# Performance work log

Hardware: AMD Instinct MI355X
Metric: run time of the kernel (lower is better)

The kernel has to match this reference:

```python
import jax, jax.numpy as jnp
import numpy as np

B, PS, H, W = 32, 1536, 32, 64
TNS = H * W                 # total_num_selects = 2048
NJ = TNS // 16              # num_joints = 128
QK = PS // 4                # q/k channels = 384
NC = 200                    # num_classes
BN_EPS = 1e-5


def setup_inputs() -> dict:
    key = jax.random.key(0)
    ks = jax.random.split(key, 8)
    s = 0.02  # small init scale for weights
    inp = {
        "x": jax.random.normal(ks[0], (B, PS, H, W), jnp.float32),
        # param_pool0: Linear(TNS -> NJ)
        "w_pool0": jax.random.normal(ks[1], (NJ, TNS), jnp.float32) * s,
        "b_pool0": jnp.zeros((NJ,), jnp.float32),
        # learnable adjacency: eye/100 + 1/100
        "adj1": jnp.eye(NJ, dtype=jnp.float32) / 100.0 + 1.0 / 100.0,
        # conv_q1 / conv_k1: Conv1d(PS -> PS//4, kernel=1)
        "w_q": jax.random.normal(ks[2], (QK, PS), jnp.float32) * s,
        "b_q": jnp.zeros((QK,), jnp.float32),
        "w_k": jax.random.normal(ks[3], (QK, PS), jnp.float32) * s,
        "b_k": jnp.zeros((QK,), jnp.float32),
        # alpha1 (torch inits to 0; we use 0.1 so attention branch has nonzero effect/grads)
        "alpha": jnp.array([0.1], jnp.float32),
        # conv1: Conv1d(PS -> PS, kernel=1)
        "w_c1": jax.random.normal(ks[4], (PS, PS), jnp.float32) * s,
        "b_c1": jnp.zeros((PS,), jnp.float32),
        # batch_norm1 affine params
        "gamma": jnp.ones((PS,), jnp.float32),
        "beta": jnp.zeros((PS,), jnp.float32),
        # param_pool1: Linear(NJ -> 1)
        "w_pool1": jax.random.normal(ks[5], (1, NJ), jnp.float32) * s,
        "b_pool1": jnp.zeros((1,), jnp.float32),
        # classifier: Linear(PS -> NC)
        "w_cls": jax.random.normal(ks[6], (NC, PS), jnp.float32) * s,
        "b_cls": jnp.zeros((NC,), jnp.float32),
    }
    return inp


def reference(x, w_pool0, b_pool0, adj1, w_q, b_q, w_k, b_k, alpha,
              w_c1, b_c1, gamma, beta, w_pool1, b_pool1, w_cls, b_cls):
    b, c = x.shape[0], x.shape[1]
    hs = x.reshape(b, c, -1)                                   # (B, PS, TNS)
    # param_pool0: pool selects down to joints
    hs = jnp.einsum('bcs,js->bcj', hs, w_pool0) + b_pool0      # (B, PS, NJ)
    # 1x1-conv q/k then mean over channel dim
    q1 = (jnp.einsum('oc,bcj->boj', w_q, hs) + b_q[:, None]).mean(axis=1)  # (B, NJ)
    k1 = (jnp.einsum('oc,bcj->boj', w_k, hs) + b_k[:, None]).mean(axis=1)  # (B, NJ)
    # outer-difference attention, tanh-bounded, blended with learnable adjacency
    A1 = adj1 + jnp.tanh(q1[:, :, None] - k1[:, None, :]) * alpha[0]       # (B, NJ, NJ)
    # conv1 (1x1) then adjacency-weighted matmul
    hs = jnp.einsum('oc,bcj->boj', w_c1, hs) + b_c1[:, None]   # (B, PS, NJ)
    hs = jnp.einsum('bcj,bjk->bck', hs, A1)                    # (B, PS, NJ)
    # BatchNorm1d over (batch, joints) per channel (training-mode batch stats)
    mean = hs.mean(axis=(0, 2))
    var = hs.var(axis=(0, 2))
    hs = (hs - mean[None, :, None]) * jax.lax.rsqrt(var + BN_EPS)[None, :, None]
    hs = gamma[None, :, None] * hs + beta[None, :, None]
    # param_pool1 (NJ -> 1), dropout is identity in eval, flatten, classify
    hs = jnp.einsum('bcj,j->bc', hs, w_pool1[0]) + b_pool1[0]  # (B, PS)
    out = hs @ w_cls.T + b_cls                                 # (B, NC)
    return out
```

## Files before the change

kernel.cpp:

```cpp
#include <hip/hip_runtime.h>
#include <hip/hip_bf16.h>

#define B_ 32
#define PS_ 1536
#define TNS_ 2048
#define NJ_ 128
#define QK_ 384
#define NC_ 200
#define BN_EPS_ 1e-5f

typedef __attribute__((ext_vector_type(8))) short short8;
typedef __attribute__((ext_vector_type(4))) float float4v;
typedef unsigned short ushort_t;

__device__ __forceinline__ unsigned short f2b(float f) {
    unsigned int u = __float_as_uint(f);
    return (unsigned short)((u + 0x7FFFu + ((u >> 16) & 1u)) >> 16);
}
__device__ __forceinline__ float b2f_lo(unsigned int u) { return __uint_as_float(u << 16); }
__device__ __forceinline__ float b2f_hi(unsigned int u) { return __uint_as_float(u & 0xffff0000u); }

__device__ __forceinline__ void mma_chunk(const short* As, const short* Bs,
                                          int wm, int wn, int lane, float4v acc[4][4]) {
    const int m0 = wm + (lane & 15);
    const int n0 = wn + (lane & 15);
    const int quad = lane >> 4;
    #pragma unroll
    for (int kk = 0; kk < 64; kk += 32) {
        short8 a[4], b[4];
        const int kb = quad * 8 + kk;
        #pragma unroll
        for (int i = 0; i < 4; ++i) {
            a[i] = *(const short8*)&As[(m0 + i * 16) * 72 + kb];
            b[i] = *(const short8*)&Bs[(n0 + i * 16) * 72 + kb];
        }
        #pragma unroll
        for (int i = 0; i < 4; ++i)
            #pragma unroll
            for (int j = 0; j < 4; ++j)
                acc[i][j] = __builtin_amdgcn_mfma_f32_16x16x32_bf16(a[i], b[j], acc[i][j], 0, 0, 0);
    }
}

__device__ __forceinline__ void stage_f32(const float* __restrict__ src, size_t stride,
                                          short* dst, int tid) {
    #pragma unroll
    for (int p = 0; p < 8; ++p) {
        int r = (tid >> 4) + p * 16;
        int kq = (tid & 15) * 4;
        float4 v = *(const float4*)(src + (size_t)r * stride + kq);
        ushort4 u = { f2b(v.x), f2b(v.y), f2b(v.z), f2b(v.w) };
        *(ushort4*)&dst[r * 72 + kq] = u;
    }
}
__device__ __forceinline__ void stage_b16(const ushort_t* __restrict__ src, size_t stride,
                                          short* dst, int tid) {
    #pragma unroll
    for (int p = 0; p < 4; ++p) {
        int r = (tid >> 3) + p * 32;
        int kq = (tid & 7) * 8;
        uint4 v = *(const uint4*)(src + (size_t)r * stride + kq);
        *(uint4*)&dst[r * 72 + kq] = v;
    }
}

__global__ void k_prep_all(const float* __restrict__ wq, const float* __restrict__ bq,
                           const float* __restrict__ wk, const float* __restrict__ bk,
                           const float* __restrict__ wp1,
                           const float* __restrict__ w0, const float* __restrict__ wc1,
                           float* __restrict__ wqb, float* __restrict__ wkb,
                           float* __restrict__ scal,
                           float* __restrict__ bnsum, float* __restrict__ bnsq,
                           ushort_t* __restrict__ w0b, ushort_t* __restrict__ wc1b) {
    const int blk = blockIdx.x;
    const int tid = threadIdx.x;
    if (blk < 6) {
        int c = blk * 256 + tid;
        float s = 0.f;
        for (int o = 0; o < QK_; ++o) s += wq[(size_t)o * PS_ + c];
        wqb[c] = s * (1.0f / QK_);
        bnsum[c] = 0.f; bnsq[c] = 0.f;
    } else if (blk < 12) {
        int c = (blk - 6) * 256 + tid;
        float s = 0.f;
        for (int o = 0; o < QK_; ++o) s += wk[(size_t)o * PS_ + c];
        wkb[c] = s * (1.0f / QK_);
    } else if (blk == 12) {
        __shared__ float red[256];
        float s = (tid < QK_ ? bq[tid] : 0.f) + (tid + 256 < QK_ ? bq[tid + 256] : 0.f);
        red[tid] = s; __syncthreads();
        for (int off = 128; off > 0; off >>= 1) { if (tid < off) red[tid] += red[tid + off]; __syncthreads(); }
        if (tid == 0) scal[0] = red[0] * (1.0f / QK_);
        __syncthreads();
        s = (tid < QK_ ? bk[tid] : 0.f) + (tid + 256 < QK_ ? bk[tid + 256] : 0.f);
        red[tid] = s; __syncthreads();
        for (int off = 128; off > 0; off >>= 1) { if (tid < off) red[tid] += red[tid + off]; __syncthreads(); }
        if (tid == 0) scal[1] = red[0] * (1.0f / QK_);
        __syncthreads();
        s = (tid < NJ_ ? wp1[tid] : 0.f);
        red[tid] = s; __syncthreads();
        for (int off = 128; off > 0; off >>= 1) { if (tid < off) red[tid] += red[tid + off]; __syncthreads(); }
        if (tid == 0) scal[2] = red[0];
    } else if (blk < 269) {
        int i = (blk - 13) * 256 + tid;
        float4 v = ((const float4*)w0)[i];
        ushort4 u = { f2b(v.x), f2b(v.y), f2b(v.z), f2b(v.w) };
        ((ushort4*)w0b)[i] = u;
    } else {
        int i = (blk - 269) * 256 + tid;
        float4 v = ((const float4*)wc1)[i];
        ushort4 u = { f2b(v.x), f2b(v.y), f2b(v.z), f2b(v.w) };
        ((ushort4*)wc1b)[i] = u;
    }
}

__global__ __launch_bounds__(256) void k_gemm1(const float* __restrict__ x,
        const ushort_t* __restrict__ w0b, const float* __restrict__ b0,
        ushort_t* __restrict__ hsT) {
    __shared__ __align__(16) short As[128 * 72];
    __shared__ __align__(16) short Bs[128 * 72];
    const int tid = threadIdx.x, lane = tid & 63, wave = tid >> 6;
    const int wm = (wave >> 1) * 64, wn = (wave & 1) * 64;
    const size_t m0 = (size_t)blockIdx.x * 128;
    float4v acc[4][4] = {};
    for (int k0 = 0; k0 < TNS_; k0 += 64) {
        stage_f32(x + m0 * TNS_ + k0, TNS_, As, tid);
        stage_b16(w0b + k0, TNS_, Bs, tid);
        __syncthreads();
        mma_chunk(As, Bs, wm, wn, lane, acc);
        __syncthreads();
    }
    const int b = blockIdx.x / 12, cb = (blockIdx.x % 12) * 128;
    const int quad = lane >> 4;
    #pragma unroll
    for (int jn = 0; jn < 4; ++jn) {
        int j = wn + jn * 16 + (lane & 15);
        float bj = b0[j];
        #pragma unroll
        for (int im = 0; im < 4; ++im) {
            int c = cb + wm + im * 16 + quad * 4;
            float4v v = acc[im][jn];
            ushort4 u = { f2b(v[0] + bj), f2b(v[1] + bj), f2b(v[2] + bj), f2b(v[3] + bj) };
            *(ushort4*)&hsT[((size_t)(b * NJ_ + j)) * PS_ + c] = u;
        }
    }
}

__global__ __launch_bounds__(256) void k_q1k1(const ushort_t* __restrict__ hsT,
        const float* __restrict__ wqb, const float* __restrict__ wkb,
        float* __restrict__ q1, float* __restrict__ k1) {
    int wid = blockIdx.x * 4 + (threadIdx.x >> 6);
    int lane = threadIdx.x & 63;
    int b = wid >> 7, j = wid & 127;
    const unsigned int* row = (const unsigned int*)(hsT + ((size_t)(b * NJ_ + j)) * PS_);
    float sq = 0.f, sk = 0.f;
    #pragma unroll
    for (int i = 0; i < 12; ++i) {
        unsigned int u = row[i * 64 + lane];
        int c = (i * 64 + lane) * 2;
        float v0 = b2f_lo(u), v1 = b2f_hi(u);
        sq += wqb[c] * v0 + wqb[c + 1] * v1;
        sk += wkb[c] * v0 + wkb[c + 1] * v1;
    }
    #pragma unroll
    for (int off = 32; off > 0; off >>= 1) { sq += __shfl_down(sq, off, 64); sk += __shfl_down(sk, off, 64); }
    if (lane == 0) { q1[b * NJ_ + j] = sq; k1[b * NJ_ + j] = sk; }
}

__global__ void k_a1(const float* __restrict__ adj, const float* __restrict__ q1,
                     const float* __restrict__ k1, const float* __restrict__ alpha,
                     const float* __restrict__ scal, ushort_t* __restrict__ A1t) {
    int idx = blockIdx.x * 256 + threadIdx.x;
    int b = idx >> 14;
    int r = idx & 16383;
    int j2 = r >> 7;
    int j = r & 127;
    float dbias = scal[0] - scal[1];
    float t = tanhf(q1[b * NJ_ + j] - k1[b * NJ_ + j2] + dbias);
    A1t[idx] = f2b(adj[j * NJ_ + j2] + t * alpha[0]);
}

__global__ __launch_bounds__(256) void k_gemm23(const ushort_t* __restrict__ wc1b,
        const float* __restrict__ bc1, const ushort_t* __restrict__ hsT,
        const ushort_t* __restrict__ A1t, ushort_t* __restrict__ hs3b,
        float* __restrict__ bnsum, float* __restrict__ bnsq) {
    __shared__ __align__(16) short sm[2][128 * 72];
    __shared__ float bns_s[NJ_], bnq_s[NJ_];
    const int tid = threadIdx.x, lane = tid & 63, wave = tid >> 6;
    const int wm = (wave >> 1) * 64, wn = (wave & 1) * 64;
    const int b = blockIdx.y, ob = blockIdx.x * 128;
    if (tid < NJ_) { bns_s[tid] = 0.f; bnq_s[tid] = 0.f; }
    float4v acc[4][4] = {};
    const ushort_t* Abase = wc1b + (size_t)ob * PS_;
    const ushort_t* Bbase = hsT + (size_t)b * NJ_ * PS_;
    for (int k0 = 0; k0 < PS_; k0 += 64) {
        stage_b16(Abase + k0, PS_, sm[0], tid);
        stage_b16(Bbase + k0, PS_, sm[1], tid);
        __syncthreads();
        mma_chunk(sm[0], sm[1], wm, wn, lane, acc);
        __syncthreads();
    }
    short* C1 = &sm[0][0];
    const int quad = lane >> 4;
    #pragma unroll
    for (int im = 0; im < 4; ++im) {
        int o0l = wm + im * 16 + quad * 4;
        float bc[4] = { bc1[ob + o0l], bc1[ob + o0l + 1], bc1[ob + o0l + 2], bc1[ob + o0l + 3] };
        #pragma unroll
        for (int jn = 0; jn < 4; ++jn) {
            int j = wn + jn * 16 + (lane & 15);
            float4v v = acc[im][jn];
            #pragma unroll
            for (int r = 0; r < 4; ++r)
                C1[(o0l + r) * 136 + j] = (short)f2b(v[r] + bc[r]);
        }
    }
    __syncthreads();
    float4v acc2[4][4] = {};
    const ushort_t* Ap = A1t + (size_t)b * NJ_ * NJ_;
    const int m0 = wm + (lane & 15), n0 = wn + (lane & 15);
    #pragma unroll
    for (int kk = 0; kk < 128; kk += 32) {
        short8 a[4], bf[4];
        const int kb = quad * 8 + kk;
        #pragma unroll
        for (int i = 0; i < 4; ++i) a[i] = *(const short8*)&C1[(m0 + i * 16) * 136 + kb];
        #pragma unroll
        for (int j = 0; j < 4; ++j) bf[j] = *(const short8*)&Ap[(size_t)(n0 + j * 16) * NJ_ + kb];
        #pragma unroll
        for (int i = 0; i < 4; ++i)
            #pragma unroll
            for (int j = 0; j < 4; ++j)
                acc2[i][j] = __builtin_amdgcn_mfma_f32_16x16x32_bf16(a[i], bf[j], acc2[i][j], 0, 0, 0);
    }
    float s_[4][4] = {}, q_[4][4] = {};
    #pragma unroll
    for (int im = 0; im < 4; ++im) {
        int c0l = wm + im * 16 + quad * 4;
        #pragma unroll
        for (int jn = 0; jn < 4; ++jn) {
            int j2 = wn + jn * 16 + (lane & 15);
            float4v v = acc2[im][jn];
            #pragma unroll
            for (int r = 0; r < 4; ++r) {
                unsigned short us = f2b(v[r]);
                float vr = b2f_lo((unsigned int)us);
                s_[im][r] += vr; q_[im][r] += vr * vr;
                hs3b[((size_t)(b * PS_) + ob + c0l + r) * NJ_ + j2] = us;
            }
        }
    }
    #pragma unroll
    for (int m = 1; m < 16; m <<= 1) {
        #pragma unroll
        for (int im = 0; im < 4; ++im)
            #pragma unroll
            for (int r = 0; r < 4; ++r) {
                s_[im][r] += __shfl_xor(s_[im][r], m, 64);
                q_[im][r] += __shfl_xor(q_[im][r], m, 64);
            }
    }
    if ((lane & 15) == 0) {
        #pragma unroll
        for (int im = 0; im < 4; ++im)
            #pragma unroll
            for (int r = 0; r < 4; ++r) {
                int cl = wm + im * 16 + quad * 4 + r;
                atomicAdd(&bns_s[cl], s_[im][r]);
                atomicAdd(&bnq_s[cl], q_[im][r]);
            }
    }
    __syncthreads();
    if (tid < NJ_) {
        atomicAdd(&bnsum[ob + tid], bns_s[tid]);
        atomicAdd(&bnsq[ob + tid], bnq_s[tid]);
    }
}

__global__ void k_pool(const ushort_t* __restrict__ hs3b, const float* __restrict__ bnsum,
                       const float* __restrict__ bnsq, const float* __restrict__ gamma,
                       const float* __restrict__ beta, const float* __restrict__ wp1,
                       const float* __restrict__ bp1, const float* __restrict__ scal,
                       float* __restrict__ p) {
    int gid = blockIdx.x * 256 + threadIdx.x;
    int row = gid >> 6;
    int lane = gid & 63;
    int c = row % PS_;
    const unsigned int* hp = (const unsigned int*)(hs3b + (size_t)row * NJ_);
    unsigned int u = hp[lane];
    float d = wp1[2 * lane] * b2f_lo(u) + wp1[2 * lane + 1] * b2f_hi(u);
    #pragma unroll
    for (int off = 32; off > 0; off >>= 1) d += __shfl_down(d, off, 64);
    if (lane == 0) {
        float mean = bnsum[c] * (1.0f / 4096.0f);
        float var = bnsq[c] * (1.0f / 4096.0f) - mean * mean;
        float s = gamma[c] * rsqrtf(var + BN_EPS_);
        p[row] = s * d + (beta[c] - s * mean) * scal[2] + bp1[0];
    }
}

__global__ void k_cls(const float* __restrict__ p, const float* __restrict__ wcls,
                      const float* __restrict__ bcls, float* __restrict__ out) {
    int gid = blockIdx.x * 256 + threadIdx.x;
    int w = gid >> 6;
    int lane = gid & 63;
    int b = w / 200, n = w % 200;
    const float* pp = p + (size_t)b * PS_;
    const float* wp = wcls + (size_t)n * PS_;
    float s = 0.f;
    for (int c = lane; c < PS_; c += 64) s += pp[c] * wp[c];
    #pragma unroll
    for (int off = 32; off > 0; off >>= 1) s += __shfl_down(s, off, 64);
    if (lane == 0) out[w] = s + bcls[n];
}

extern "C" void kernel_launch(void* const* d_in, const int* in_sizes, int n_in,
                              void* d_out, int out_size, void* d_ws, size_t ws_size,
                              hipStream_t stream) {
    const float* x       = (const float*)d_in[0];
    const float* w_pool0 = (const float*)d_in[1];
    const float* b_pool0 = (const float*)d_in[2];
    const float* adj1    = (const float*)d_in[3];
    const float* w_q     = (const float*)d_in[4];
    const float* b_q     = (const float*)d_in[5];
    const float* w_k     = (const float*)d_in[6];
    const float* b_k     = (const float*)d_in[7];
    const float* alpha   = (const float*)d_in[8];
    const float* w_c1    = (const float*)d_in[9];
    const float* b_c1    = (const float*)d_in[10];
    const float* gamma   = (const float*)d_in[11];
    const float* beta    = (const float*)d_in[12];
    const float* w_pool1 = (const float*)d_in[13];
    const float* b_pool1 = (const float*)d_in[14];
    const float* w_cls   = (const float*)d_in[15];
    const float* b_cls   = (const float*)d_in[16];
    float* out = (float*)d_out;

    ushort_t* hsT  = (ushort_t*)d_ws;
    ushort_t* hs2  = hsT + 6291456;
    ushort_t* hs3b = hs2 + 6291456;
    ushort_t* w0b  = hs3b + 6291456;
    ushort_t* wc1b = w0b + 262144;
    ushort_t* A1t  = wc1b + 2359296;
    float* fb    = (float*)(A1t + 524288);
    float* wqb   = fb;
    float* wkb   = wqb + 1536;
    float* scal  = wkb + 1536;
    float* q1    = scal + 16;
    float* k1    = q1 + 4096;
    float* bnsum = k1 + 4096;
    float* bnsq  = bnsum + 1536;
    float* pbuf  = bnsq + 1536;
    size_t need = 44040192u + (size_t)(1536 + 1536 + 16 + 4096 + 4096 + 1536 + 1536 + 49152) * 4;
    if (ws_size < need) return;

    k_prep_all<<<2573, 256, 0, stream>>>(w_q, b_q, w_k, b_k, w_pool1, w_pool0, w_c1,
                                         wqb, wkb, scal, bnsum, bnsq, w0b, wc1b);
    k_gemm1 <<<384, 256, 0, stream>>>(x, w0b, b_pool0, hsT);
    k_q1k1  <<<1024, 256, 0, stream>>>(hsT, wqb, wkb, q1, k1);
    k_a1    <<<2048, 256, 0, stream>>>(adj1, q1, k1, alpha, scal, A1t);
    k_gemm23<<<dim3(12, 32), 256, 0, stream>>>(wc1b, b_c1, hsT, A1t, hs3b, bnsum, bnsq);
    k_pool  <<<12288, 256, 0, stream>>>(hs3b, bnsum, bnsq, gamma, beta, w_pool1, b_pool1, scal, pbuf);
    k_cls   <<<1600, 256, 0, stream>>>(pbuf, w_cls, b_cls, out);
}
```

Before: 677.6 us.

## Fuse q/k reduction into gemm1 and pooling into gemm23, use 512-thread blocks

The q1/k1 channel-mean dot products move into the gemm1 epilogue, accumulated with atomics into buffers that the prep kernel now zeroes. The wp1-weighted pooling moves into the gemm23 epilogue, so the bf16 hs3 tensor is no longer written and read back, and the BN affine is applied inside the classifier. Both GEMMs now launch 8 waves per block with a 4x2 MFMA tile per wave, halving each wave's accumulator footprint. In exchange, the q1/k1 sums become atomic-order nondeterministic and k_cls recomputes the BN scale for every output.

```diff
diff --git a/kernel.cpp b/kernel.cpp
--- a/kernel.cpp
+++ b/kernel.cpp
@@ -20,44 +20,43 @@
 __device__ __forceinline__ float b2f_lo(unsigned int u) { return __uint_as_float(u << 16); }
 __device__ __forceinline__ float b2f_hi(unsigned int u) { return __uint_as_float(u & 0xffff0000u); }
 
-__device__ __forceinline__ void mma_chunk(const short* As, const short* Bs,
-                                          int wm, int wn, int lane, float4v acc[4][4]) {
+__device__ __forceinline__ void mma_chunk42(const short* As, const short* Bs,
+                                            int wm, int wn, int lane, float4v acc[4][2]) {
     const int m0 = wm + (lane & 15);
     const int n0 = wn + (lane & 15);
     const int quad = lane >> 4;
     #pragma unroll
     for (int kk = 0; kk < 64; kk += 32) {
-        short8 a[4], b[4];
+        short8 a[4], b[2];
         const int kb = quad * 8 + kk;
         #pragma unroll
-        for (int i = 0; i < 4; ++i) {
-            a[i] = *(const short8*)&As[(m0 + i * 16) * 72 + kb];
-            b[i] = *(const short8*)&Bs[(n0 + i * 16) * 72 + kb];
-        }
+        for (int i = 0; i < 4; ++i) a[i] = *(const short8*)&As[(m0 + i * 16) * 72 + kb];
+        #pragma unroll
+        for (int j = 0; j < 2; ++j) b[j] = *(const short8*)&Bs[(n0 + j * 16) * 72 + kb];
         #pragma unroll
         for (int i = 0; i < 4; ++i)
             #pragma unroll
-            for (int j = 0; j < 4; ++j)
+            for (int j = 0; j < 2; ++j)
                 acc[i][j] = __builtin_amdgcn_mfma_f32_16x16x32_bf16(a[i], b[j], acc[i][j], 0, 0, 0);
     }
 }
 
-__device__ __forceinline__ void stage_f32(const float* __restrict__ src, size_t stride,
-                                          short* dst, int tid) {
-    #pragma unroll
-    for (int p = 0; p < 8; ++p) {
-        int r = (tid >> 4) + p * 16;
+__device__ __forceinline__ void stage_f32_512(const float* __restrict__ src, size_t stride,
+                                              short* dst, int tid) {
+    #pragma unroll
+    for (int p = 0; p < 4; ++p) {
+        int r = (tid >> 4) + p * 32;
         int kq = (tid & 15) * 4;
         float4 v = *(const float4*)(src + (size_t)r * stride + kq);
         ushort4 u = { f2b(v.x), f2b(v.y), f2b(v.z), f2b(v.w) };
         *(ushort4*)&dst[r * 72 + kq] = u;
     }
 }
-__device__ __forceinline__ void stage_b16(const ushort_t* __restrict__ src, size_t stride,
-                                          short* dst, int tid) {
-    #pragma unroll
-    for (int p = 0; p < 4; ++p) {
-        int r = (tid >> 3) + p * 32;
+__device__ __forceinline__ void stage_b16_512(const ushort_t* __restrict__ src, size_t stride,
+                                              short* dst, int tid) {
+    #pragma unroll
+    for (int p = 0; p < 2; ++p) {
+        int r = (tid >> 3) + p * 64;
         int kq = (tid & 7) * 8;
         uint4 v = *(const uint4*)(src + (size_t)r * stride + kq);
         *(uint4*)&dst[r * 72 + kq] = v;
@@ -71,6 +70,7 @@
                            float* __restrict__ wqb, float* __restrict__ wkb,
                            float* __restrict__ scal,
                            float* __restrict__ bnsum, float* __restrict__ bnsq,
+                           float* __restrict__ q1, float* __restrict__ k1,
                            ushort_t* __restrict__ w0b, ushort_t* __restrict__ wc1b) {
     const int blk = blockIdx.x;
     const int tid = threadIdx.x;
@@ -106,65 +106,70 @@
         float4 v = ((const float4*)w0)[i];
         ushort4 u = { f2b(v.x), f2b(v.y), f2b(v.z), f2b(v.w) };
         ((ushort4*)w0b)[i] = u;
-    } else {
+    } else if (blk < 2573) {
         int i = (blk - 269) * 256 + tid;
         float4 v = ((const float4*)wc1)[i];
         ushort4 u = { f2b(v.x), f2b(v.y), f2b(v.z), f2b(v.w) };
         ((ushort4*)wc1b)[i] = u;
-    }
-}
-
-__global__ __launch_bounds__(256) void k_gemm1(const float* __restrict__ x,
+    } else {
+        int i = (blk - 2573) * 256 + tid;
+        if (i < 4096) q1[i] = 0.f; else k1[i - 4096] = 0.f;
+    }
+}
+
+__global__ __launch_bounds__(512) void k_gemm1(const float* __restrict__ x,
         const ushort_t* __restrict__ w0b, const float* __restrict__ b0,
-        ushort_t* __restrict__ hsT) {
+        const float* __restrict__ wqb, const float* __restrict__ wkb,
+        ushort_t* __restrict__ hsT, float* __restrict__ q1, float* __restrict__ k1) {
     __shared__ __align__(16) short As[128 * 72];
     __shared__ __align__(16) short Bs[128 * 72];
     const int tid = threadIdx.x, lane = tid & 63, wave = tid >> 6;
-    const int wm = (wave >> 1) * 64, wn = (wave & 1) * 64;
-    const size_t m0 = (size_t)blockIdx.x * 128;
-    float4v acc[4][4] = {};
+    const int wm = (wave >> 2) * 64, wn = (wave & 3) * 32;
+    const size_t m0r = (size_t)blockIdx.x * 128;
+    float4v acc[4][2] = {};
     for (int k0 = 0; k0 < TNS_; k0 += 64) {
-        stage_f32(x + m0 * TNS_ + k0, TNS_, As, tid);
-        stage_b16(w0b + k0, TNS_, Bs, tid);
-        __syncthreads();
-        mma_chunk(As, Bs, wm, wn, lane, acc);
+        stage_f32_512(x + m0r * TNS_ + k0, TNS_, As, tid);
+        stage_b16_512(w0b + k0, TNS_, Bs, tid);
+        __syncthreads();
+        mma_chunk42(As, Bs, wm, wn, lane, acc);
         __syncthreads();
     }
     const int b = blockIdx.x / 12, cb = (blockIdx.x % 12) * 128;
-    const int quad = lane >> 4;
-    #pragma unroll
-    for (int jn = 0; jn < 4; ++jn) {
-        int j = wn + jn * 16 + (lane & 15);
+    const int quad = lane >> 4, s = lane & 15;
+    float sq[2] = { 0.f, 0.f }, sk[2] = { 0.f, 0.f };
+    #pragma unroll
+    for (int jn = 0; jn < 2; ++jn) {
+        int j = wn + jn * 16 + s;
         float bj = b0[j];
         #pragma unroll
         for (int im = 0; im < 4; ++im) {
             int c = cb + wm + im * 16 + quad * 4;
             float4v v = acc[im][jn];
-            ushort4 u = { f2b(v[0] + bj), f2b(v[1] + bj), f2b(v[2] + bj), f2b(v[3] + bj) };
+            unsigned short us[4];
+            #pragma unroll
+            for (int r = 0; r < 4; ++r) {
+                us[r] = f2b(v[r] + bj);
+                float vr = b2f_lo((unsigned int)us[r]);
+                sq[jn] += wqb[c + r] * vr;
+                sk[jn] += wkb[c + r] * vr;
+            }
+            ushort4 u = { us[0], us[1], us[2], us[3] };
             *(ushort4*)&hsT[((size_t)(b * NJ_ + j)) * PS_ + c] = u;
         }
     }
-}
-
-__global__ __launch_bounds__(256) void k_q1k1(const ushort_t* __restrict__ hsT,
-        const float* __restrict__ wqb, const float* __restrict__ wkb,
-        float* __restrict__ q1, float* __restrict__ k1) {
-    int wid = blockIdx.x * 4 + (threadIdx.x >> 6);
-    int lane = threadIdx.x & 63;
-    int b = wid >> 7, j = wid & 127;
-    const unsigned int* row = (const unsigned int*)(hsT + ((size_t)(b * NJ_ + j)) * PS_);
-    float sq = 0.f, sk = 0.f;
-    #pragma unroll
-    for (int i = 0; i < 12; ++i) {
-        unsigned int u = row[i * 64 + lane];
-        int c = (i * 64 + lane) * 2;
-        float v0 = b2f_lo(u), v1 = b2f_hi(u);
-        sq += wqb[c] * v0 + wqb[c + 1] * v1;
-        sk += wkb[c] * v0 + wkb[c + 1] * v1;
-    }
-    #pragma unroll
-    for (int off = 32; off > 0; off >>= 1) { sq += __shfl_down(sq, off, 64); sk += __shfl_down(sk, off, 64); }
-    if (lane == 0) { q1[b * NJ_ + j] = sq; k1[b * NJ_ + j] = sk; }
+    #pragma unroll
+    for (int jn = 0; jn < 2; ++jn) {
+        sq[jn] += __shfl_xor(sq[jn], 16, 64); sq[jn] += __shfl_xor(sq[jn], 32, 64);
+        sk[jn] += __shfl_xor(sk[jn], 16, 64); sk[jn] += __shfl_xor(sk[jn], 32, 64);
+    }
+    if (quad == 0) {
+        #pragma unroll
+        for (int jn = 0; jn < 2; ++jn) {
+            int j = wn + jn * 16 + s;
+            atomicAdd(&q1[b * NJ_ + j], sq[jn]);
+            atomicAdd(&k1[b * NJ_ + j], sk[jn]);
+        }
+    }
 }
 
 __global__ void k_a1(const float* __restrict__ adj, const float* __restrict__ q1,
@@ -180,35 +185,35 @@
     A1t[idx] = f2b(adj[j * NJ_ + j2] + t * alpha[0]);
 }
 
-__global__ __launch_bounds__(256) void k_gemm23(const ushort_t* __restrict__ wc1b,
+__global__ __launch_bounds__(512) void k_gemm23(const ushort_t* __restrict__ wc1b,
         const float* __restrict__ bc1, const ushort_t* __restrict__ hsT,
-        const ushort_t* __restrict__ A1t, ushort_t* __restrict__ hs3b,
-        float* __restrict__ bnsum, float* __restrict__ bnsq) {
+        const ushort_t* __restrict__ A1t, const float* __restrict__ wp1,
+        float* __restrict__ bnsum, float* __restrict__ bnsq, float* __restrict__ dout) {
     __shared__ __align__(16) short sm[2][128 * 72];
-    __shared__ float bns_s[NJ_], bnq_s[NJ_];
+    __shared__ float bns_s[NJ_], bnq_s[NJ_], ds_s[NJ_];
     const int tid = threadIdx.x, lane = tid & 63, wave = tid >> 6;
-    const int wm = (wave >> 1) * 64, wn = (wave & 1) * 64;
+    const int wm = (wave >> 2) * 64, wn = (wave & 3) * 32;
     const int b = blockIdx.y, ob = blockIdx.x * 128;
-    if (tid < NJ_) { bns_s[tid] = 0.f; bnq_s[tid] = 0.f; }
-    float4v acc[4][4] = {};
+    if (tid < NJ_) { bns_s[tid] = 0.f; bnq_s[tid] = 0.f; ds_s[tid] = 0.f; }
+    float4v acc[4][2] = {};
     const ushort_t* Abase = wc1b + (size_t)ob * PS_;
     const ushort_t* Bbase = hsT + (size_t)b * NJ_ * PS_;
     for (int k0 = 0; k0 < PS_; k0 += 64) {
-        stage_b16(Abase + k0, PS_, sm[0], tid);
-        stage_b16(Bbase + k0, PS_, sm[1], tid);
-        __syncthreads();
-        mma_chunk(sm[0], sm[1], wm, wn, lane, acc);
+        stage_b16_512(Abase + k0, PS_, sm[0], tid);
+        stage_b16_512(Bbase + k0, PS_, sm[1], tid);
+        __syncthreads();
+        mma_chunk42(sm[0], sm[1], wm, wn, lane, acc);
         __syncthreads();
     }
     short* C1 = &sm[0][0];
-    const int quad = lane >> 4;
+    const int quad = lane >> 4, s = lane & 15;
     #pragma unroll
     for (int im = 0; im < 4; ++im) {
         int o0l = wm + im * 16 + quad * 4;
         float bc[4] = { bc1[ob + o0l], bc1[ob + o0l + 1], bc1[ob + o0l + 2], bc1[ob + o0l + 3] };
         #pragma unroll
-        for (int jn = 0; jn < 4; ++jn) {
-            int j = wn + jn * 16 + (lane & 15);
+        for (int jn = 0; jn < 2; ++jn) {
+            int j = wn + jn * 16 + s;
             float4v v = acc[im][jn];
             #pragma unroll
             for (int r = 0; r < 4; ++r)
@@ -216,102 +221,86 @@
         }
     }
     __syncthreads();
-    float4v acc2[4][4] = {};
+    float4v acc2[4][2] = {};
     const ushort_t* Ap = A1t + (size_t)b * NJ_ * NJ_;
-    const int m0 = wm + (lane & 15), n0 = wn + (lane & 15);
+    const int m0 = wm + s, n0 = wn + s;
     #pragma unroll
     for (int kk = 0; kk < 128; kk += 32) {
-        short8 a[4], bf[4];
+        short8 a[4], bf[2];
         const int kb = quad * 8 + kk;
         #pragma unroll
         for (int i = 0; i < 4; ++i) a[i] = *(const short8*)&C1[(m0 + i * 16) * 136 + kb];
         #pragma unroll
-        for (int j = 0; j < 4; ++j) bf[j] = *(const short8*)&Ap[(size_t)(n0 + j * 16) * NJ_ + kb];
+        for (int j = 0; j < 2; ++j) bf[j] = *(const short8*)&Ap[(size_t)(n0 + j * 16) * NJ_ + kb];
         #pragma unroll
         for (int i = 0; i < 4; ++i)
             #pragma unroll
-            for (int j = 0; j < 4; ++j)
+            for (int j = 0; j < 2; ++j)
                 acc2[i][j] = __builtin_amdgcn_mfma_f32_16x16x32_bf16(a[i], bf[j], acc2[i][j], 0, 0, 0);
     }
-    float s_[4][4] = {}, q_[4][4] = {};
     #pragma unroll
     for (int im = 0; im < 4; ++im) {
-        int c0l = wm + im * 16 + quad * 4;
-        #pragma unroll
-        for (int jn = 0; jn < 4; ++jn) {
-            int j2 = wn + jn * 16 + (lane & 15);
+        float s4[4] = {}, q4[4] = {}, d4[4] = {};
+        #pragma unroll
+        for (int jn = 0; jn < 2; ++jn) {
+            int j2 = wn + jn * 16 + s;
+            float w1 = wp1[j2];
             float4v v = acc2[im][jn];
             #pragma unroll
             for (int r = 0; r < 4; ++r) {
-                unsigned short us = f2b(v[r]);
-                float vr = b2f_lo((unsigned int)us);
-                s_[im][r] += vr; q_[im][r] += vr * vr;
-                hs3b[((size_t)(b * PS_) + ob + c0l + r) * NJ_ + j2] = us;
+                float vr = b2f_lo((unsigned int)f2b(v[r]));
+                s4[r] += vr; q4[r] += vr * vr; d4[r] += w1 * vr;
             }
         }
-    }
-    #pragma unroll
-    for (int m = 1; m < 16; m <<= 1) {
-        #pragma unroll
-        for (int im = 0; im < 4; ++im)
+        #pragma unroll
+        for (int m = 1; m < 16; m <<= 1)
             #pragma unroll
             for (int r = 0; r < 4; ++r) {
-                s_[im][r] += __shfl_xor(s_[im][r], m, 64);
-                q_[im][r] += __shfl_xor(q_[im][r], m, 64);
+                s4[r] += __shfl_xor(s4[r], m, 64);
+                q4[r] += __shfl_xor(q4[r], m, 64);
+                d4[r] += __shfl_xor(d4[r], m, 64);
             }
-    }
-    if ((lane & 15) == 0) {
-        #pragma unroll
-        for (int im = 0; im < 4; ++im)
+        if (s == 0) {
             #pragma unroll
             for (int r = 0; r < 4; ++r) {
                 int cl = wm + im * 16 + quad * 4 + r;
-                atomicAdd(&bns_s[cl], s_[im][r]);
-                atomicAdd(&bnq_s[cl], q_[im][r]);
+                atomicAdd(&bns_s[cl], s4[r]);
+                atomicAdd(&bnq_s[cl], q4[r]);
+                atomicAdd(&ds_s[cl], d4[r]);
             }
+        }
     }
     __syncthreads();
     if (tid < NJ_) {
         atomicAdd(&bnsum[ob + tid], bns_s[tid]);
         atomicAdd(&bnsq[ob + tid], bnq_s[tid]);
-    }
-}
-
-__global__ void k_pool(const ushort_t* __restrict__ hs3b, const float* __restrict__ bnsum,
-                       const float* __restrict__ bnsq, const float* __restrict__ gamma,
-                       const float* __restrict__ beta, const float* __restrict__ wp1,
-                       const float* __restrict__ bp1, const float* __restrict__ scal,
-                       float* __restrict__ p) {
-    int gid = blockIdx.x * 256 + threadIdx.x;
-    int row = gid >> 6;
-    int lane = gid & 63;
-    int c = row % PS_;
-    const unsigned int* hp = (const unsigned int*)(hs3b + (size_t)row * NJ_);
-    unsigned int u = hp[lane];
-    float d = wp1[2 * lane] * b2f_lo(u) + wp1[2 * lane + 1] * b2f_hi(u);
-    #pragma unroll
-    for (int off = 32; off > 0; off >>= 1) d += __shfl_down(d, off, 64);
-    if (lane == 0) {
-        float mean = bnsum[c] * (1.0f / 4096.0f);
-        float var = bnsq[c] * (1.0f / 4096.0f) - mean * mean;
-        float s = gamma[c] * rsqrtf(var + BN_EPS_);
-        p[row] = s * d + (beta[c] - s * mean) * scal[2] + bp1[0];
-    }
-}
-
-__global__ void k_cls(const float* __restrict__ p, const float* __restrict__ wcls,
+        dout[(size_t)b * PS_ + ob + tid] = ds_s[tid];
+    }
+}
+
+__global__ void k_cls(const float* __restrict__ dout, const float* __restrict__ bnsum,
+                      const float* __restrict__ bnsq, const float* __restrict__ gamma,
+                      const float* __restrict__ beta, const float* __restrict__ scal,
+                      const float* __restrict__ bp1, const float* __restrict__ wcls,
                       const float* __restrict__ bcls, float* __restrict__ out) {
     int gid = blockIdx.x * 256 + threadIdx.x;
     int w = gid >> 6;
     int lane = gid & 63;
     int b = w / 200, n = w % 200;
-    const float* pp = p + (size_t)b * PS_;
+    const float* dp = dout + (size_t)b * PS_;
     const float* wp = wcls + (size_t)n * PS_;
-    float s = 0.f;
-    for (int c = lane; c < PS_; c += 64) s += pp[c] * wp[c];
-    #pragma unroll
-    for (int off = 32; off > 0; off >>= 1) s += __shfl_down(s, off, 64);
-    if (lane == 0) out[w] = s + bcls[n];
+    float sc2 = scal[2], bb = bp1[0];
+    float acc = 0.f;
+    for (int c = lane; c < PS_; c += 64) {
+        float mean = bnsum[c] * (1.0f / 4096.0f);
+        float var = bnsq[c] * (1.0f / 4096.0f) - mean * mean;
+        float sc = gamma[c] * rsqrtf(var + BN_EPS_);
+        float pval = sc * dp[c] + (beta[c] - sc * mean) * sc2 + bb;
+        acc += wp[c] * pval;
+    }
+    #pragma unroll
+    for (int off = 32; off > 0; off >>= 1) acc += __shfl_down(acc, off, 64);
+    if (lane == 0) out[w] = acc + bcls[n];
 }
 
 extern "C" void kernel_launch(void* const* d_in, const int* in_sizes, int n_in,
@@ -350,16 +339,16 @@
     float* k1    = q1 + 4096;
     float* bnsum = k1 + 4096;
     float* bnsq  = bnsum + 1536;
-    float* pbuf  = bnsq + 1536;
+    float* dbuf  = bnsq + 1536;
     size_t need = 44040192u + (size_t)(1536 + 1536 + 16 + 4096 + 4096 + 1536 + 1536 + 49152) * 4;
     if (ws_size < need) return;
 
-    k_prep_all<<<2573, 256, 0, stream>>>(w_q, b_q, w_k, b_k, w_pool1, w_pool0, w_c1,
-                                         wqb, wkb, scal, bnsum, bnsq, w0b, wc1b);
-    k_gemm1 <<<384, 256, 0, stream>>>(x, w0b, b_pool0, hsT);
-    k_q1k1  <<<1024, 256, 0, stream>>>(hsT, wqb, wkb, q1, k1);
+    k_prep_all<<<2605, 256, 0, stream>>>(w_q, b_q, w_k, b_k, w_pool1, w_pool0, w_c1,
+                                         wqb, wkb, scal, bnsum, bnsq, q1, k1, w0b, wc1b);
+    k_gemm1 <<<384, 512, 0, stream>>>(x, w0b, b_pool0, wqb, wkb, hsT, q1, k1);
     k_a1    <<<2048, 256, 0, stream>>>(adj1, q1, k1, alpha, scal, A1t);
-    k_gemm23<<<dim3(12, 32), 256, 0, stream>>>(wc1b, b_c1, hsT, A1t, hs3b, bnsum, bnsq);
-    k_pool  <<<12288, 256, 0, stream>>>(hs3b, bnsum, bnsq, gamma, beta, w_pool1, b_pool1, scal, pbuf);
-    k_cls   <<<1600, 256, 0, stream>>>(pbuf, w_cls, b_cls, out);
-}
+    k_gemm23<<<dim3(12, 32), 512, 0, stream>>>(wc1b, b_c1, hsT, A1t, w_pool1,
+                                               bnsum, bnsq, dbuf);
+    k_cls   <<<1600, 256, 0, stream>>>(dbuf, bnsum, bnsq, gamma, beta, scal,
+                                       b_pool1, w_cls, b_cls, out);
+}
```

Result: no change. 667.8 us (-1.4%).
